# Performance work log

Measured on AMD Instinct MI355X. Metric: run time of the kernel, lower is better.

Reference implementation:

```python
import jax, jax.numpy as jnp
import numpy as np

N_NODES = 100000
N_EDGES = 1600000
F_IN = 128
HEADS = 4
C_OUT = 32
NEG_SLOPE = 0.2


def setup_inputs() -> dict:
    key = jax.random.key(0)
    k1, k2, k3, k4, k5, k6 = jax.random.split(key, 6)
    x = jax.random.normal(k1, (N_NODES, F_IN), dtype=jnp.float32)
    edge_index = jax.random.randint(k2, (2, N_EDGES), 0, N_NODES, dtype=jnp.int64)
    # glorot-ish scales
    W = jax.random.normal(k3, (F_IN, HEADS * C_OUT), dtype=jnp.float32) * (1.0 / np.sqrt(F_IN))
    att_src = jax.random.normal(k4, (HEADS, C_OUT), dtype=jnp.float32) * (1.0 / np.sqrt(C_OUT))
    att_dst = jax.random.normal(k5, (HEADS, C_OUT), dtype=jnp.float32) * (1.0 / np.sqrt(C_OUT))
    bias = jnp.zeros((HEADS * C_OUT,), dtype=jnp.float32)
    return {"x": x, "edge_index": edge_index, "W": W,
            "att_src": att_src, "att_dst": att_dst, "bias": bias}


def _gat_forward(x, edge_index, W, att_src, att_dst, bias):
    N = x.shape[0]
    H, C = att_src.shape
    h = (x @ W).reshape(N, H, C)                      # [N,H,C]
    # PyG GATConv default: add self-loops
    loops = jnp.arange(N, dtype=edge_index.dtype)
    src = jnp.concatenate([edge_index[0], loops])     # [E+N]
    dst = jnp.concatenate([edge_index[1], loops])
    a_src = jnp.einsum("nhc,hc->nh", h, att_src)      # [N,H]
    a_dst = jnp.einsum("nhc,hc->nh", h, att_dst)
    e = jax.nn.leaky_relu(a_src[src] + a_dst[dst], NEG_SLOPE)  # [E+N,H]
    # segment softmax over destination node (every node has a self-loop)
    m = jax.ops.segment_max(e, dst, num_segments=N)
    e = jnp.exp(e - m[dst])
    s = jax.ops.segment_sum(e, dst, num_segments=N)
    alpha = e / (s[dst] + 1e-16)                      # [E+N,H]
    msg = h[src] * alpha[:, :, None]                  # [E+N,H,C]
    out = jax.ops.segment_sum(msg, dst, num_segments=N).reshape(N, H * C)
    return jnp.tanh(out + bias)


def reference(x, edge_index, W, att_src, att_dst, bias):
    return _gat_forward(x, edge_index, W, att_src, att_dst, bias)
```

## Files before the change

### kernel.cpp

```cpp
#include <hip/hip_runtime.h>
#include <math.h>

#define NN 100000
#define NE 1600000
#define F_IN 128
#define HEADS 4
#define HC 128
#define NEG_SLOPE 0.2f
#define NBKT 391
#define NSCAT 391
#define BCAP 5120
#define LDK 136
#define NSTRIP 6250

typedef __attribute__((ext_vector_type(8))) short bf16x8;
typedef __attribute__((ext_vector_type(4))) float f32x4;
typedef __attribute__((ext_vector_type(2))) float f32x2;

static __device__ __forceinline__ short f2bf_rne(float f) {
    unsigned u = __float_as_uint(f);
    unsigned r = (u + 0x7FFFu + ((u >> 16) & 1u)) >> 16;
    return (short)r;
}
static __device__ __forceinline__ float bf2f(short s) {
    return __uint_as_float(((unsigned)(unsigned short)s) << 16);
}

static __device__ __forceinline__ void pk_fma(f32x2& d, f32x2 a, f32x2 b) {
    asm("v_pk_fma_f32 %0, %1, %2, %0 op_sel:[0,0,0] op_sel_hi:[1,1,1]"
        : "+v"(d) : "v"(a), "v"(b));
}
static __device__ __forceinline__ void pk_add(f32x2& d, f32x2 a) {
    asm("v_pk_add_f32 %0, %1, %0 op_sel:[0,0] op_sel_hi:[1,1]"
        : "+v"(d) : "v"(a));
}
static __device__ __forceinline__ f32x2 mkpair(float a, float b) {
    f32x2 r; r.x = a; r.y = b; return r;
}

__global__ __launch_bounds__(256) void prep_kernel(
        const float* __restrict__ W, short* __restrict__ wt_hi, short* __restrict__ wt_lo,
        const int* __restrict__ ei, int* __restrict__ flag) {
    if (blockIdx.x == 0 && threadIdx.x < 64) {
        int l = threadIdx.x;
        int v = ei[2 * l + 1];
        for (int off = 1; off < 64; off <<= 1) v |= __shfl_xor(v, off);
        if (l == 0) *flag = (v == 0) ? 1 : 0;
    }
    int i = blockIdx.x * 256 + threadIdx.x;
    if (i >= F_IN * HC) return;
    int k = i >> 7, n = i & 127;
    float f = W[k * HC + n];
    short hb = f2bf_rne(f);
    wt_hi[n * F_IN + k] = hb;
    wt_lo[n * F_IN + k] = f2bf_rne(f - bf2f(hb));
}

__global__ __launch_bounds__(256, 4) void fused_gemm_scatter_kernel(
        const float* __restrict__ x, const short* __restrict__ wt_hi,
        const short* __restrict__ wt_lo, const float* __restrict__ att_src,
        const float* __restrict__ att_dst, unsigned short* __restrict__ h_bf,
        float* __restrict__ a_src, float* __restrict__ a_dst,
        const int* __restrict__ ei, const int* __restrict__ flag,
        int* __restrict__ bcur, unsigned* __restrict__ pairs) {
    __shared__ union SM {
        struct { short hi[64 * LDK]; short lo[64 * LDK]; } w;
        struct { int lhist[NBKT]; int gbase[NBKT]; } b;
    } sm;
    int t = threadIdx.x;

    if (blockIdx.x < NSCAT) {
        for (int i = t; i < NBKT; i += 256) sm.b.lhist[i] = 0;
        __syncthreads();
        int is64 = *flag;
        int base = blockIdx.x * 4096;

        unsigned wrd[16];
        int meta[16];
#pragma unroll
        for (int it = 0; it < 16; ++it) {
            int e = base + it * 256 + t;
            if (e < NE) {
                int src = is64 ? ei[2 * e] : ei[e];
                int dst = is64 ? ei[2 * NE + 2 * e] : ei[NE + e];
                int b = dst >> 8;
                int r = atomicAdd(&sm.b.lhist[b], 1);
                wrd[it] = (unsigned)src | ((unsigned)(dst & 255) << 17);
                meta[it] = b | (r << 9);
            } else {
                meta[it] = -1;
            }
        }
        __syncthreads();
        for (int i = t; i < NBKT; i += 256)
            sm.b.gbase[i] = sm.b.lhist[i] ? atomicAdd(&bcur[i], sm.b.lhist[i]) : 0;
        __syncthreads();
#pragma unroll
        for (int it = 0; it < 16; ++it) {
            if (meta[it] >= 0) {
                int b = meta[it] & 511;
                int r = meta[it] >> 9;
                pairs[(size_t)b * BCAP + sm.b.gbase[b] + r] = wrd[it];
            }
        }
        return;
    }

    int blk = blockIdx.x - NSCAT;

    for (int c = t; c < 1024; c += 256) {
        int n = c >> 4;
        int kk = (c & 15) * 8;
        *(bf16x8*)(sm.w.hi + n * LDK + kk) = *(const bf16x8*)(wt_hi + n * F_IN + kk);
        *(bf16x8*)(sm.w.lo + n * LDK + kk) = *(const bf16x8*)(wt_lo + n * F_IN + kk);
    }
    __syncthreads();

    int strip = blk * 4 + (t >> 6);
    int valid = strip < NSTRIP;
    int sclamp = valid ? strip : NSTRIP - 1;
    int lane = t & 63;
    int l15 = lane & 15;
    int q = lane >> 4;

    f32x4 acc[8];
#pragma unroll
    for (int nt = 0; nt < 8; ++nt) acc[nt] = (f32x4){0.f, 0.f, 0.f, 0.f};

    bf16x8 ah[4], al[4];
    const float* xp = x + (size_t)(sclamp * 16 + l15) * F_IN + q * 8;

#pragma unroll
    for (int ki = 0; ki < 4; ++ki) {
        float4 v0 = *(const float4*)(xp + ki * 32);
        float4 v1 = *(const float4*)(xp + ki * 32 + 4);
        float vv[8] = {v0.x, v0.y, v0.z, v0.w, v1.x, v1.y, v1.z, v1.w};
#pragma unroll
        for (int j = 0; j < 8; ++j) {
            short hb = f2bf_rne(vv[j]);
            ah[ki][j] = hb;
            al[ki][j] = f2bf_rne(vv[j] - bf2f(hb));
        }
        int koff = ki * 32 + q * 8;
#pragma unroll
        for (int nt = 0; nt < 4; ++nt) {
            int lidx = (nt * 16 + l15) * LDK + koff;
            bf16x8 b_hi = *(const bf16x8*)(sm.w.hi + lidx);
            bf16x8 b_lo = *(const bf16x8*)(sm.w.lo + lidx);
            acc[nt] = __builtin_amdgcn_mfma_f32_16x16x32_bf16(ah[ki], b_hi, acc[nt], 0, 0, 0);
            acc[nt] = __builtin_amdgcn_mfma_f32_16x16x32_bf16(al[ki], b_hi, acc[nt], 0, 0, 0);
            acc[nt] = __builtin_amdgcn_mfma_f32_16x16x32_bf16(ah[ki], b_lo, acc[nt], 0, 0, 0);
        }
    }

    __syncthreads();
    for (int c = t; c < 1024; c += 256) {
        int n = c >> 4;
        int kk = (c & 15) * 8;
        *(bf16x8*)(sm.w.hi + n * LDK + kk) = *(const bf16x8*)(wt_hi + (64 + n) * F_IN + kk);
        *(bf16x8*)(sm.w.lo + n * LDK + kk) = *(const bf16x8*)(wt_lo + (64 + n) * F_IN + kk);
    }
    __syncthreads();

#pragma unroll
    for (int ki = 0; ki < 4; ++ki) {
        int koff = ki * 32 + q * 8;
#pragma unroll
        for (int nt = 0; nt < 4; ++nt) {
            int lidx = (nt * 16 + l15) * LDK + koff;
            bf16x8 b_hi = *(const bf16x8*)(sm.w.hi + lidx);
            bf16x8 b_lo = *(const bf16x8*)(sm.w.lo + lidx);
            acc[4 + nt] = __builtin_amdgcn_mfma_f32_16x16x32_bf16(ah[ki], b_hi, acc[4 + nt], 0, 0, 0);
            acc[4 + nt] = __builtin_amdgcn_mfma_f32_16x16x32_bf16(al[ki], b_hi, acc[4 + nt], 0, 0, 0);
            acc[4 + nt] = __builtin_amdgcn_mfma_f32_16x16x32_bf16(ah[ki], b_lo, acc[4 + nt], 0, 0, 0);
        }
    }

    if (!valid) return;

    int orow = strip * 16 + q * 4;
#pragma unroll
    for (int nt = 0; nt < 8; ++nt)
#pragma unroll
        for (int r = 0; r < 4; ++r)
            h_bf[(size_t)(orow + r) * HC + nt * 16 + l15] =
                (unsigned short)f2bf_rne(acc[nt][r]);

#pragma unroll
    for (int hd = 0; hd < 4; ++hd) {
        float as0 = att_src[hd * 32 + l15];
        float as1 = att_src[hd * 32 + 16 + l15];
        float ad0 = att_dst[hd * 32 + l15];
        float ad1 = att_dst[hd * 32 + 16 + l15];
#pragma unroll
        for (int r = 0; r < 4; ++r) {
            float ps = acc[2 * hd][r] * as0 + acc[2 * hd + 1][r] * as1;
            float pd = acc[2 * hd][r] * ad0 + acc[2 * hd + 1][r] * ad1;
#pragma unroll
            for (int off = 1; off < 16; off <<= 1) {
                ps += __shfl_xor(ps, off);
                pd += __shfl_xor(pd, off);
            }
            if (l15 == 0) {
                int row = orow + r;
                a_src[row * 4 + hd] = ps;
                a_dst[row * 4 + hd] = pd;
            }
        }
    }
}

__global__ __launch_bounds__(256) void bucket_csr_kernel(
        const int* __restrict__ bcur, const unsigned* __restrict__ pairs,
        const float* __restrict__ a_src, const float* __restrict__ a_dst,
        int* __restrict__ deg, int* __restrict__ offsets,
        int* __restrict__ csr_src, unsigned* __restrict__ wal) {
    __shared__ unsigned lpairs[BCAP];
    __shared__ int sd[256];
    __shared__ int cnt256[256];
    __shared__ int lcur[256];

    int b = blockIdx.x;
    int t = threadIdx.x;
    int node = (b << 8) + t;

    int partial = 0;
    for (int i = t; i < b; i += 256) partial += bcur[i];
    sd[t] = partial;
    __syncthreads();
    for (int off = 128; off > 0; off >>= 1) {
        if (t < off) sd[t] += sd[t + off];
        __syncthreads();
    }
    int bktbase = sd[0];
    __syncthreads();

    cnt256[t] = 0;
    __syncthreads();

    int cnt = bcur[b];
    const unsigned* __restrict__ bp = pairs + (size_t)b * BCAP;
    for (int i = t; i < cnt; i += 256) {
        unsigned w = bp[i];
        lpairs[i] = w;
        atomicAdd(&cnt256[w >> 17], 1);
    }
    __syncthreads();

    int v = cnt256[t];
    sd[t] = v;
    __syncthreads();
    for (int off = 1; off < 256; off <<= 1) {
        int u = (t >= off) ? sd[t - off] : 0;
        __syncthreads();
        sd[t] += u;
        __syncthreads();
    }
    int myoff = bktbase + sd[t] - v;
    if (node < NN) {
        deg[node] = v;
        offsets[node] = myoff;
    }
    lcur[t] = myoff;
    __syncthreads();

    for (int i = t; i < cnt; i += 256) {
        unsigned w = lpairs[i];
        int src = (int)(w & 0x1FFFFu);
        int dl = (int)(w >> 17);
        float4 as = ((const float4*)a_src)[src];
        float4 ad = ((const float4*)a_dst)[(b << 8) + dl];
        float e0 = as.x + ad.x; e0 = (e0 < 0.f) ? NEG_SLOPE * e0 : e0;
        float e1 = as.y + ad.y; e1 = (e1 < 0.f) ? NEG_SLOPE * e1 : e1;
        float e2 = as.z + ad.z; e2 = (e2 < 0.f) ? NEG_SLOPE * e2 : e2;
        float e3 = as.w + ad.w; e3 = (e3 < 0.f) ? NEG_SLOPE * e3 : e3;
        float w0 = __expf(e0), w1 = __expf(e1), w2 = __expf(e2), w3 = __expf(e3);
        int pos = atomicAdd(&lcur[dl], 1);
        csr_src[pos] = src;
        unsigned lo = (unsigned)(unsigned short)f2bf_rne(w0) |
                      ((unsigned)(unsigned short)f2bf_rne(w1) << 16);
        unsigned hi = (unsigned)(unsigned short)f2bf_rne(w2) |
                      ((unsigned)(unsigned short)f2bf_rne(w3) << 16);
        ((uint2*)wal)[pos] = make_uint2(lo, hi);
    }
}

__global__ __launch_bounds__(256) void gat_aggr_kernel(
        const int* __restrict__ offsets, const int* __restrict__ deg,
        const int* __restrict__ csr_src, const unsigned* __restrict__ wal,
        const float* __restrict__ a_src, const float* __restrict__ a_dst,
        const unsigned* __restrict__ h2, const float* __restrict__ bias,
        float* __restrict__ out) {
    int wid = (blockIdx.x * 256 + threadIdx.x) >> 6;
    int dst = __builtin_amdgcn_readfirstlane(wid);
    if (dst >= NN) return;
    int lane = threadIdx.x & 63;
    int hd = lane >> 4;
    unsigned hsel2 = (unsigned)(hd & 2);
    unsigned shamt = (hd & 1) ? 0u : 16u;

    int start = offsets[dst];
    int n = deg[dst];

    f32x2 accx2 = {0.f, 0.f}, accy2 = {0.f, 0.f}, ws2 = {0.f, 0.f};

    int j = 0;
    for (; j + 7 < n; j += 8) {
        int base = start + j;
        int s0 = csr_src[base + 0];
        int s1 = csr_src[base + 1];
        int s2 = csr_src[base + 2];
        int s3 = csr_src[base + 3];
        int s4 = csr_src[base + 4];
        int s5 = csr_src[base + 5];
        int s6 = csr_src[base + 6];
        int s7 = csr_src[base + 7];
        uint2 wv0 = ((const uint2*)wal)[base + 0];
        uint2 wv1 = ((const uint2*)wal)[base + 1];
        uint2 wv2 = ((const uint2*)wal)[base + 2];
        uint2 wv3 = ((const uint2*)wal)[base + 3];
        uint2 wv4 = ((const uint2*)wal)[base + 4];
        uint2 wv5 = ((const uint2*)wal)[base + 5];
        uint2 wv6 = ((const uint2*)wal)[base + 6];
        uint2 wv7 = ((const uint2*)wal)[base + 7];
        unsigned u0 = h2[(size_t)s0 * 64 + lane];
        unsigned u1 = h2[(size_t)s1 * 64 + lane];
        unsigned u2 = h2[(size_t)s2 * 64 + lane];
        unsigned u3 = h2[(size_t)s3 * 64 + lane];
        unsigned u4 = h2[(size_t)s4 * 64 + lane];
        unsigned u5 = h2[(size_t)s5 * 64 + lane];
        unsigned u6 = h2[(size_t)s6 * 64 + lane];
        unsigned u7 = h2[(size_t)s7 * 64 + lane];
#define EDGEPAIR(ua, ub, wva, wvb)                                              \
        {                                                                       \
            unsigned wsa = hsel2 ? wva.y : wva.x;                               \
            unsigned wsb = hsel2 ? wvb.y : wvb.x;                               \
            f32x2 wp = mkpair(__uint_as_float((wsa << shamt) & 0xFFFF0000u),    \
                              __uint_as_float((wsb << shamt) & 0xFFFF0000u));   \
            f32x2 hx = mkpair(__uint_as_float(ua << 16),                        \
                              __uint_as_float(ub << 16));                       \
            f32x2 hy = mkpair(__uint_as_float(ua & 0xFFFF0000u),                \
                              __uint_as_float(ub & 0xFFFF0000u));               \
            pk_add(ws2, wp);                                                    \
            pk_fma(accx2, wp, hx);                                              \
            pk_fma(accy2, wp, hy);                                              \
        }
        EDGEPAIR(u0, u1, wv0, wv1)
        EDGEPAIR(u2, u3, wv2, wv3)
        EDGEPAIR(u4, u5, wv4, wv5)
        EDGEPAIR(u6, u7, wv6, wv7)
    }
    for (; j + 1 < n; j += 2) {
        int base = start + j;
        int s0 = csr_src[base + 0];
        int s1 = csr_src[base + 1];
        uint2 wv0 = ((const uint2*)wal)[base + 0];
        uint2 wv1 = ((const uint2*)wal)[base + 1];
        unsigned u0 = h2[(size_t)s0 * 64 + lane];
        unsigned u1 = h2[(size_t)s1 * 64 + lane];
        EDGEPAIR(u0, u1, wv0, wv1)
    }
#undef EDGEPAIR
    float accx = accx2.x + accx2.y;
    float accy = accy2.x + accy2.y;
    float wsum = ws2.x + ws2.y;
    if (j < n) {
        int base = start + j;
        int s0 = csr_src[base];
        uint2 wv0 = ((const uint2*)wal)[base];
        unsigned u0 = h2[(size_t)s0 * 64 + lane];
        unsigned ws0 = hsel2 ? wv0.y : wv0.x;
        float w0 = __uint_as_float((ws0 << shamt) & 0xFFFF0000u);
        wsum += w0;
        accx += w0 * __uint_as_float(u0 << 16);
        accy += w0 * __uint_as_float(u0 & 0xFFFF0000u);
    }

    float e = a_src[dst * 4 + hd] + a_dst[dst * 4 + hd];
    e = (e < 0.f) ? NEG_SLOPE * e : e;
    float sf = __expf(e);
    float inv = 1.f / (wsum + sf + 1e-16f);

    unsigned us = h2[(size_t)dst * 64 + lane];
    float2 b2 = ((const float2*)bias)[lane];
    float ox = tanhf((accx + sf * __uint_as_float(us << 16)) * inv + b2.x);
    float oy = tanhf((accy + sf * __uint_as_float(us & 0xFFFF0000u)) * inv + b2.y);
    ((float2*)out)[(size_t)dst * 64 + lane] = make_float2(ox, oy);
}

extern "C" void kernel_launch(void* const* d_in, const int* in_sizes, int n_in,
                              void* d_out, int out_size, void* d_ws, size_t ws_size,
                              hipStream_t stream) {
    const float* x       = (const float*)d_in[0];
    const int*   ei      = (const int*)  d_in[1];
    const float* W       = (const float*)d_in[2];
    const float* att_src = (const float*)d_in[3];
    const float* att_dst = (const float*)d_in[4];
    const float* bias    = (const float*)d_in[5];
    float* out = (float*)d_out;

    unsigned short* h_bf = (unsigned short*)d_ws;
    float* a_src = (float*)(h_bf + (size_t)NN * HC);
    float* a_dst = a_src + (size_t)NN * HEADS;
    short* wt_hi = (short*)(a_dst + (size_t)NN * HEADS);
    short* wt_lo = wt_hi + F_IN * HC;
    int* flag    = (int*)(wt_lo + F_IN * HC);
    int* bcur    = flag + 4;
    int* deg     = bcur + NBKT + 1;
    int* offsets = deg + NN;
    int* csr_src = offsets + NN;
    unsigned* wal = (unsigned*)(csr_src + NE);
    unsigned* pairs = (unsigned*)(wal + (size_t)NE * 2);

    hipMemsetAsync(bcur, 0, NBKT * sizeof(int), stream);

    hipLaunchKernelGGL(prep_kernel, dim3(64), dim3(256), 0, stream,
                       W, wt_hi, wt_lo, ei, flag);

    hipLaunchKernelGGL(fused_gemm_scatter_kernel, dim3(NSCAT + 1563), dim3(256), 0, stream,
                       x, wt_hi, wt_lo, att_src, att_dst, h_bf, a_src, a_dst,
                       ei, flag, bcur, pairs);

    hipLaunchKernelGGL(bucket_csr_kernel, dim3(NBKT), dim3(256), 0, stream,
                       bcur, pairs, a_src, a_dst, deg, offsets, csr_src, wal);

    hipLaunchKernelGGL(gat_aggr_kernel, dim3(NN * 64 / 256), dim3(256), 0, stream,
                       offsets, deg, csr_src, wal, a_src, a_dst,
                       (const unsigned*)h_bf, bias, out);
}
```

Baseline: 263.5 us.

## Split fused GEMM/scatter, use finer 64-node buckets with direct global atomics

Splits the fused GEMM-plus-edge-scatter kernel into two kernels. The scatter now bins edges into 1563 buckets of 64 destination nodes using per-edge global atomics instead of LDS histograms with block-level reservation. The GEMM uses 512-thread blocks and packed bf16 conversion instructions. The bucket CSR kernel is adapted to 64-node buckets with smaller LDS, which gives more blocks and better balance. The price is heavier global atomic contention, an extra kernel launch, and the loss of the overlap between GEMM and scatter.

Result: slower. 459.2 us (+74.3%).

```diff
diff --git a/kernel.cpp b/kernel.cpp
--- a/kernel.cpp
+++ b/kernel.cpp
@@ -7,9 +7,8 @@
 #define HEADS 4
 #define HC 128
 #define NEG_SLOPE 0.2f
-#define NBKT 391
-#define NSCAT 391
-#define BCAP 5120
+#define NBKT 1563
+#define BCAP 1280
 #define LDK 136
 #define NSTRIP 6250
 
@@ -24,6 +23,11 @@
 }
 static __device__ __forceinline__ float bf2f(short s) {
     return __uint_as_float(((unsigned)(unsigned short)s) << 16);
+}
+static __device__ __forceinline__ unsigned cvt_pk_bf16(float a, float b) {
+    unsigned r;
+    asm("v_cvt_pk_bf16_f32 %0, %1, %2" : "=v"(r) : "v"(a), "v"(b));
+    return r;
 }
 
 static __device__ __forceinline__ void pk_fma(f32x2& d, f32x2 a, f32x2 b) {
@@ -56,67 +60,44 @@
     wt_lo[n * F_IN + k] = f2bf_rne(f - bf2f(hb));
 }
 
-__global__ __launch_bounds__(256, 4) void fused_gemm_scatter_kernel(
+__global__ __launch_bounds__(256) void scatter_kernel(
+        const int* __restrict__ ei, const int* __restrict__ flag,
+        int* __restrict__ bcur, unsigned* __restrict__ pairs) {
+    int t = threadIdx.x;
+    int is64 = *flag;
+    int base = blockIdx.x * 1024;
+#pragma unroll
+    for (int it = 0; it < 4; ++it) {
+        int e = base + it * 256 + t;
+        if (e < NE) {
+            int src = is64 ? ei[2 * e] : ei[e];
+            int dst = is64 ? ei[2 * NE + 2 * e] : ei[NE + e];
+            int b = dst >> 6;
+            int r = atomicAdd(&bcur[b], 1);
+            pairs[(size_t)b * BCAP + r] = (unsigned)src | ((unsigned)(dst & 63) << 17);
+        }
+    }
+}
+
+__global__ __launch_bounds__(512) void mfma_gemm_kernel(
         const float* __restrict__ x, const short* __restrict__ wt_hi,
         const short* __restrict__ wt_lo, const float* __restrict__ att_src,
         const float* __restrict__ att_dst, unsigned short* __restrict__ h_bf,
-        float* __restrict__ a_src, float* __restrict__ a_dst,
-        const int* __restrict__ ei, const int* __restrict__ flag,
-        int* __restrict__ bcur, unsigned* __restrict__ pairs) {
-    __shared__ union SM {
-        struct { short hi[64 * LDK]; short lo[64 * LDK]; } w;
-        struct { int lhist[NBKT]; int gbase[NBKT]; } b;
-    } sm;
+        float* __restrict__ a_src, float* __restrict__ a_dst) {
+    __shared__ short lw_hi[64 * LDK];
+    __shared__ short lw_lo[64 * LDK];
     int t = threadIdx.x;
-
-    if (blockIdx.x < NSCAT) {
-        for (int i = t; i < NBKT; i += 256) sm.b.lhist[i] = 0;
-        __syncthreads();
-        int is64 = *flag;
-        int base = blockIdx.x * 4096;
-
-        unsigned wrd[16];
-        int meta[16];
-#pragma unroll
-        for (int it = 0; it < 16; ++it) {
-            int e = base + it * 256 + t;
-            if (e < NE) {
-                int src = is64 ? ei[2 * e] : ei[e];
-                int dst = is64 ? ei[2 * NE + 2 * e] : ei[NE + e];
-                int b = dst >> 8;
-                int r = atomicAdd(&sm.b.lhist[b], 1);
-                wrd[it] = (unsigned)src | ((unsigned)(dst & 255) << 17);
-                meta[it] = b | (r << 9);
-            } else {
-                meta[it] = -1;
-            }
-        }
-        __syncthreads();
-        for (int i = t; i < NBKT; i += 256)
-            sm.b.gbase[i] = sm.b.lhist[i] ? atomicAdd(&bcur[i], sm.b.lhist[i]) : 0;
-        __syncthreads();
-#pragma unroll
-        for (int it = 0; it < 16; ++it) {
-            if (meta[it] >= 0) {
-                int b = meta[it] & 511;
-                int r = meta[it] >> 9;
-                pairs[(size_t)b * BCAP + sm.b.gbase[b] + r] = wrd[it];
-            }
-        }
-        return;
-    }
-
-    int blk = blockIdx.x - NSCAT;
-
-    for (int c = t; c < 1024; c += 256) {
+    int blk = blockIdx.x;
+
+    for (int c = t; c < 1024; c += 512) {
         int n = c >> 4;
         int kk = (c & 15) * 8;
-        *(bf16x8*)(sm.w.hi + n * LDK + kk) = *(const bf16x8*)(wt_hi + n * F_IN + kk);
-        *(bf16x8*)(sm.w.lo + n * LDK + kk) = *(const bf16x8*)(wt_lo + n * F_IN + kk);
-    }
-    __syncthreads();
-
-    int strip = blk * 4 + (t >> 6);
+        *(bf16x8*)(lw_hi + n * LDK + kk) = *(const bf16x8*)(wt_hi + n * F_IN + kk);
+        *(bf16x8*)(lw_lo + n * LDK + kk) = *(const bf16x8*)(wt_lo + n * F_IN + kk);
+    }
+    __syncthreads();
+
+    int strip = blk * 8 + (t >> 6);
     int valid = strip < NSTRIP;
     int sclamp = valid ? strip : NSTRIP - 1;
     int lane = t & 63;
@@ -127,7 +108,8 @@
 #pragma unroll
     for (int nt = 0; nt < 8; ++nt) acc[nt] = (f32x4){0.f, 0.f, 0.f, 0.f};
 
-    bf16x8 ah[4], al[4];
+    union BU { bf16x8 v; unsigned u[4]; };
+    BU ah[4], al[4];
     const float* xp = x + (size_t)(sclamp * 16 + l15) * F_IN + q * 8;
 
 #pragma unroll
@@ -136,29 +118,32 @@
         float4 v1 = *(const float4*)(xp + ki * 32 + 4);
         float vv[8] = {v0.x, v0.y, v0.z, v0.w, v1.x, v1.y, v1.z, v1.w};
 #pragma unroll
-        for (int j = 0; j < 8; ++j) {
-            short hb = f2bf_rne(vv[j]);
-            ah[ki][j] = hb;
-            al[ki][j] = f2bf_rne(vv[j] - bf2f(hb));
+        for (int j = 0; j < 4; ++j) {
+            float f0 = vv[2 * j], f1 = vv[2 * j + 1];
+            unsigned hp = cvt_pk_bf16(f0, f1);
+            ah[ki].u[j] = hp;
+            float r0 = f0 - __uint_as_float(hp << 16);
+            float r1 = f1 - __uint_as_float(hp & 0xFFFF0000u);
+            al[ki].u[j] = cvt_pk_bf16(r0, r1);
         }
         int koff = ki * 32 + q * 8;
 #pragma unroll
         for (int nt = 0; nt < 4; ++nt) {
             int lidx = (nt * 16 + l15) * LDK + koff;
-            bf16x8 b_hi = *(const bf16x8*)(sm.w.hi + lidx);
-            bf16x8 b_lo = *(const bf16x8*)(sm.w.lo + lidx);
-            acc[nt] = __builtin_amdgcn_mfma_f32_16x16x32_bf16(ah[ki], b_hi, acc[nt], 0, 0, 0);
-            acc[nt] = __builtin_amdgcn_mfma_f32_16x16x32_bf16(al[ki], b_hi, acc[nt], 0, 0, 0);
-            acc[nt] = __builtin_amdgcn_mfma_f32_16x16x32_bf16(ah[ki], b_lo, acc[nt], 0, 0, 0);
-        }
-    }
-
-    __syncthreads();
-    for (int c = t; c < 1024; c += 256) {
+            bf16x8 b_hi = *(const bf16x8*)(lw_hi + lidx);
+            bf16x8 b_lo = *(const bf16x8*)(lw_lo + lidx);
+            acc[nt] = __builtin_amdgcn_mfma_f32_16x16x32_bf16(ah[ki].v, b_hi, acc[nt], 0, 0, 0);
+            acc[nt] = __builtin_amdgcn_mfma_f32_16x16x32_bf16(al[ki].v, b_hi, acc[nt], 0, 0, 0);
+            acc[nt] = __builtin_amdgcn_mfma_f32_16x16x32_bf16(ah[ki].v, b_lo, acc[nt], 0, 0, 0);
+        }
+    }
+
+    __syncthreads();
+    for (int c = t; c < 1024; c += 512) {
         int n = c >> 4;
         int kk = (c & 15) * 8;
-        *(bf16x8*)(sm.w.hi + n * LDK + kk) = *(const bf16x8*)(wt_hi + (64 + n) * F_IN + kk);
-        *(bf16x8*)(sm.w.lo + n * LDK + kk) = *(const bf16x8*)(wt_lo + (64 + n) * F_IN + kk);
+        *(bf16x8*)(lw_hi + n * LDK + kk) = *(const bf16x8*)(wt_hi + (64 + n) * F_IN + kk);
+        *(bf16x8*)(lw_lo + n * LDK + kk) = *(const bf16x8*)(wt_lo + (64 + n) * F_IN + kk);
     }
     __syncthreads();
 
@@ -168,11 +153,11 @@
 #pragma unroll
         for (int nt = 0; nt < 4; ++nt) {
             int lidx = (nt * 16 + l15) * LDK + koff;
-            bf16x8 b_hi = *(const bf16x8*)(sm.w.hi + lidx);
-            bf16x8 b_lo = *(const bf16x8*)(sm.w.lo + lidx);
-            acc[4 + nt] = __builtin_amdgcn_mfma_f32_16x16x32_bf16(ah[ki], b_hi, acc[4 + nt], 0, 0, 0);
-            acc[4 + nt] = __builtin_amdgcn_mfma_f32_16x16x32_bf16(al[ki], b_hi, acc[4 + nt], 0, 0, 0);
-            acc[4 + nt] = __builtin_amdgcn_mfma_f32_16x16x32_bf16(ah[ki], b_lo, acc[4 + nt], 0, 0, 0);
+            bf16x8 b_hi = *(const bf16x8*)(lw_hi + lidx);
+            bf16x8 b_lo = *(const bf16x8*)(lw_lo + lidx);
+            acc[4 + nt] = __builtin_amdgcn_mfma_f32_16x16x32_bf16(ah[ki].v, b_hi, acc[4 + nt], 0, 0, 0);
+            acc[4 + nt] = __builtin_amdgcn_mfma_f32_16x16x32_bf16(al[ki].v, b_hi, acc[4 + nt], 0, 0, 0);
+            acc[4 + nt] = __builtin_amdgcn_mfma_f32_16x16x32_bf16(ah[ki].v, b_lo, acc[4 + nt], 0, 0, 0);
         }
     }
 
@@ -217,12 +202,11 @@
         int* __restrict__ csr_src, unsigned* __restrict__ wal) {
     __shared__ unsigned lpairs[BCAP];
     __shared__ int sd[256];
-    __shared__ int cnt256[256];
-    __shared__ int lcur[256];
+    __shared__ int cnt64[64];
+    __shared__ int lcur[64];
 
     int b = blockIdx.x;
     int t = threadIdx.x;
-    int node = (b << 8) + t;
 
     int partial = 0;
     for (int i = t; i < b; i += 256) partial += bcur[i];
@@ -235,7 +219,7 @@
     int bktbase = sd[0];
     __syncthreads();
 
-    cnt256[t] = 0;
+    if (t < 64) cnt64[t] = 0;
     __syncthreads();
 
     int cnt = bcur[b];
@@ -243,25 +227,29 @@
     for (int i = t; i < cnt; i += 256) {
         unsigned w = bp[i];
         lpairs[i] = w;
-        atomicAdd(&cnt256[w >> 17], 1);
-    }
-    __syncthreads();
-
-    int v = cnt256[t];
-    sd[t] = v;
-    __syncthreads();
-    for (int off = 1; off < 256; off <<= 1) {
-        int u = (t >= off) ? sd[t - off] : 0;
+        atomicAdd(&cnt64[w >> 17], 1);
+    }
+    __syncthreads();
+
+    if (t < 64) sd[t] = cnt64[t];
+    __syncthreads();
+    for (int off = 1; off < 64; off <<= 1) {
+        int u = 0;
+        if (t < 64 && t >= off) u = sd[t - off];
         __syncthreads();
-        sd[t] += u;
+        if (t < 64) sd[t] += u;
         __syncthreads();
     }
-    int myoff = bktbase + sd[t] - v;
-    if (node < NN) {
-        deg[node] = v;
-        offsets[node] = myoff;
-    }
-    lcur[t] = myoff;
+    if (t < 64) {
+        int v = cnt64[t];
+        int myoff = bktbase + sd[t] - v;
+        int node = (b << 6) + t;
+        if (node < NN) {
+            deg[node] = v;
+            offsets[node] = myoff;
+        }
+        lcur[t] = myoff;
+    }
     __syncthreads();
 
     for (int i = t; i < cnt; i += 256) {
@@ -269,7 +257,7 @@
         int src = (int)(w & 0x1FFFFu);
         int dl = (int)(w >> 17);
         float4 as = ((const float4*)a_src)[src];
-        float4 ad = ((const float4*)a_dst)[(b << 8) + dl];
+        float4 ad = ((const float4*)a_dst)[(b << 6) + dl];
         float e0 = as.x + ad.x; e0 = (e0 < 0.f) ? NEG_SLOPE * e0 : e0;
         float e1 = as.y + ad.y; e1 = (e1 < 0.f) ? NEG_SLOPE * e1 : e1;
         float e2 = as.z + ad.z; e2 = (e2 < 0.f) ? NEG_SLOPE * e2 : e2;
@@ -417,9 +405,11 @@
     hipLaunchKernelGGL(prep_kernel, dim3(64), dim3(256), 0, stream,
                        W, wt_hi, wt_lo, ei, flag);
 
-    hipLaunchKernelGGL(fused_gemm_scatter_kernel, dim3(NSCAT + 1563), dim3(256), 0, stream,
-                       x, wt_hi, wt_lo, att_src, att_dst, h_bf, a_src, a_dst,
+    hipLaunchKernelGGL(scatter_kernel, dim3((NE + 1023) / 1024), dim3(256), 0, stream,
                        ei, flag, bcur, pairs);
+
+    hipLaunchKernelGGL(mfma_gemm_kernel, dim3(782), dim3(512), 0, stream,
+                       x, wt_hi, wt_lo, att_src, att_dst, h_bf, a_src, a_dst);
 
     hipLaunchKernelGGL(bucket_csr_kernel, dim3(NBKT), dim3(256), 0, stream,
                        bcur, pairs, a_src, a_dst, deg, offsets, csr_src, wal);
```
